# Kernel tuning notes

Hardware: AMD Instinct MI355X
Metric: run time of the kernel (lower is better)

## Reference

```python
import jax, jax.numpy as jnp
import numpy as np

N = 20000   # nodes
E = 320000  # edges
H = 4       # attention heads
GAT_SLOPE = 0.2   # DGL GATv2Conv internal leaky_relu slope
ACT_SLOPE = 0.01  # nn.LeakyReLU default slope


def gatv2_layer(h, src, dst, Wl, Wr, attn, b):
    """DGL GATv2Conv (share_weights=False, bias=True, eval mode).
    h: [N, Fin]; Wl/Wr: [Fin, H*D]; attn: [H, D]; b: [H*D]. Returns [N, H, D]."""
    n = h.shape[0]
    Hh, D = attn.shape
    fs = (h @ Wl).reshape(n, Hh, D)  # source projection
    fd = (h @ Wr).reshape(n, Hh, D)  # destination projection
    # edge-wise GATv2 score: a^T leaky_relu(Wl h_u + Wr h_v)
    e = jax.nn.leaky_relu(fs[src] + fd[dst], negative_slope=GAT_SLOPE)  # [E,H,D]
    logit = jnp.einsum('ehd,hd->eh', e, attn)  # [E,H]
    # edge softmax over incoming edges of each dst node (numerically stable)
    m = jax.ops.segment_max(logit, dst, num_segments=n)
    a = jnp.exp(logit - m[dst])
    s = jax.ops.segment_sum(a, dst, num_segments=n)
    alpha = a / s[dst]  # [E,H]
    out = jax.ops.segment_sum(alpha[:, :, None] * fs[src], dst, num_segments=n)
    return out + b.reshape(1, Hh, D)


def setup_inputs() -> dict:
    key = jax.random.key(0)
    ks = jax.random.split(key, 16)

    def w(k, shape, fan_in):
        return (jax.random.normal(k, shape, jnp.float32) / np.float32(np.sqrt(fan_in)))

    return {
        'n_feat': jax.random.normal(ks[0], (N, 512), jnp.float32),
        'src': jax.random.randint(ks[1], (E,), 0, N, jnp.int32),
        'dst': jax.random.randint(ks[2], (E,), 0, N, jnp.int32),
        # layer 0: 512 -> H x 128
        'Wl0': w(ks[3], (512, H * 128), 512), 'Wr0': w(ks[4], (512, H * 128), 512),
        'attn0': w(ks[5], (H, 128), 128), 'b0': jnp.zeros((H * 128,), jnp.float32),
        # layer 1: 128 -> H x 128
        'Wl1': w(ks[6], (128, H * 128), 128), 'Wr1': w(ks[7], (128, H * 128), 128),
        'attn1': w(ks[8], (H, 128), 128), 'b1': jnp.zeros((H * 128,), jnp.float32),
        # layer 2 (output): 128 -> H x 64
        'Wl2': w(ks[9], (128, H * 64), 128), 'Wr2': w(ks[10], (128, H * 64), 128),
        'attn2': w(ks[11], (H, 64), 64), 'b2': jnp.zeros((H * 64,), jnp.float32),
    }


def reference(n_feat, src, dst, Wl0, Wr0, attn0, b0, Wl1, Wr1, attn1, b1,
              Wl2, Wr2, attn2, b2):
    h = n_feat.reshape(n_feat.shape[0], -1)  # nn.Flatten
    for (Wl, Wr, attn, b) in ((Wl0, Wr0, attn0, b0),
                              (Wl1, Wr1, attn1, b1),
                              (Wl2, Wr2, attn2, b2)):
        h = gatv2_layer(h, src, dst, Wl, Wr, attn, b)  # [N,H,D]
        h = h.mean(axis=1)                              # head mean
        h = jax.nn.leaky_relu(h, negative_slope=ACT_SLOPE)
    # dgl.mean_nodes: per-graph mean readout (single graph -> [1, out])
    return h.mean(axis=0, keepdims=True)
```

## Files before the change

### kernel.cpp

```cpp
#include <hip/hip_runtime.h>
#include <hip/hip_bf16.h>
#include <stdint.h>


#define GAT_SLOPE 0.2f
#define ACT_SLOPE 0.01f
#define MAXDEG 64

typedef _Float16 half8 __attribute__((ext_vector_type(8)));
typedef _Float16 v2h __attribute__((ext_vector_type(2)));
typedef float floatx4 __attribute__((ext_vector_type(4)));

struct TransDesc {
  const float* src;
  _Float16* dst;
  int K, M, off;
};
struct PreArgs {
  TransDesc d[9];
  int wTotal;
  const float* nf;
  _Float16* A0;
  int aTotal;
  const int* src;
  const int* dst;
  int* counts;
  int* pcsrc;
  int E;
};

__global__ __launch_bounds__(256) void preproc_kernel(PreArgs pa) {
  int i = blockIdx.x * 256 + threadIdx.x;
  const int total = pa.wTotal + pa.aTotal + pa.E;
  if (i >= total) return;
  if (i < pa.wTotal) {
    int q = 0;
#pragma unroll
    for (int j = 1; j < 9; ++j)
      if (i >= pa.d[j].off) q = j;
    int local = i - pa.d[q].off;
    int K = pa.d[q].K, M = pa.d[q].M;
    int m = local / K, k = local % K;
    pa.d[q].dst[local] = (_Float16)pa.d[q].src[(size_t)k * M + m];
  } else if (i < pa.wTotal + pa.aTotal) {
    int j = i - pa.wTotal;
    pa.A0[j] = (_Float16)pa.nf[j];
  } else {
    int e = i - pa.wTotal - pa.aTotal;
    int d = pa.dst[e];
    int pos = atomicAdd(&pa.counts[d], 1);
    if (pos < MAXDEG) pa.pcsrc[(size_t)d * MAXDEG + pos] = pa.src[e];
  }
}

__device__ __forceinline__ void gload_lds16(const _Float16* g, _Float16* l) {
  __builtin_amdgcn_global_load_lds(
      (__attribute__((address_space(1))) unsigned int*)g,
      (__attribute__((address_space(3))) unsigned int*)l, 16, 0, 0);
}

#define TM 128
#define TN 128
#define TK 32

__global__ __launch_bounds__(256) void gemm_mfma_dual_kernel(
    const _Float16* __restrict__ A, const _Float16* __restrict__ B0,
    const _Float16* __restrict__ B1, _Float16* __restrict__ C0,
    _Float16* __restrict__ C1, int Nrow, int K, int M, int nStrips,
    int nbxLog2) {
  const int id = blockIdx.x;
  const int xcd = id & 7;
  const int s = id >> 3;
  const int nbx = 1 << nbxLog2;
  const int col = s & (nbx - 1);
  const int chunk = s >> nbxLog2;
  const int strip = chunk * 8 + xcd;
  if (strip >= nStrips) return;

  const int nb = nbx >> 1;
  const bool second = col >= nb;
  const _Float16* B = second ? B1 : B0;
  _Float16* C = second ? C1 : C0;
  const int bn = (second ? col - nb : col) * TN;
  const int bm = strip * TM;

  __shared__ __align__(16) _Float16 As[TM * TK];
  __shared__ __align__(16) _Float16 Bs[TN * TK];

  const int tid = threadIdx.x;
  const int w = tid >> 6;
  const int lane = tid & 63;
  const int wr = w >> 1;
  const int wc = w & 1;
  const int quad = lane >> 4;
  const int lr = lane & 15;

  const int lrow = lane >> 2;
  const int loff = (lane & 3) * 8;

  floatx4 acc[4][4];
#pragma unroll
  for (int i = 0; i < 4; ++i)
#pragma unroll
    for (int j = 0; j < 4; ++j) acc[i][j] = (floatx4){0.f, 0.f, 0.f, 0.f};

  const int KT = K / TK;
  for (int kt = 0; kt < KT; ++kt) {
    const int k0 = kt * TK;
#pragma unroll
    for (int half = 0; half < 2; ++half) {
      const int r0 = w * 32 + half * 16;
      int ga = bm + r0 + lrow;
      if (ga >= Nrow) ga = Nrow - 1;
      gload_lds16(A + (size_t)ga * K + k0 + loff, As + r0 * TK);
      gload_lds16(B + (size_t)(bn + r0 + lrow) * K + k0 + loff, Bs + r0 * TK);
    }
    __syncthreads();

    half8 ar[4], br[4];
#pragma unroll
    for (int i = 0; i < 4; ++i) {
      int row = wr * 64 + i * 16 + lr;
      ar[i] = *(const half8*)(As + row * TK + quad * 8);
    }
#pragma unroll
    for (int j = 0; j < 4; ++j) {
      int colr = wc * 64 + j * 16 + lr;
      br[j] = *(const half8*)(Bs + colr * TK + quad * 8);
    }
#pragma unroll
    for (int i = 0; i < 4; ++i)
#pragma unroll
      for (int j = 0; j < 4; ++j)
        acc[i][j] = __builtin_amdgcn_mfma_f32_16x16x32_f16(ar[i], br[j],
                                                           acc[i][j], 0, 0, 0);
    __syncthreads();
  }

#pragma unroll
  for (int i = 0; i < 4; ++i) {
#pragma unroll
    for (int r = 0; r < 4; ++r) {
      int row = bm + wr * 64 + i * 16 + quad * 4 + r;
      if (row >= Nrow) continue;
#pragma unroll
      for (int j = 0; j < 4; ++j) {
        int colc = bn + wc * 64 + j * 16 + lr;
        C[(size_t)row * M + colc] = (_Float16)acc[i][j][r];
      }
    }
  }
}

template <int CTRL>
__device__ __forceinline__ float dpp_add(float x) {
  int y = __builtin_amdgcn_update_dpp(0, __builtin_bit_cast(int, x), CTRL,
                                      0xF, 0xF, true);
  return x + __builtin_bit_cast(float, y);
}
__device__ __forceinline__ float row_sum16(float x) {
  x = dpp_add<0x121>(x);
  x = dpp_add<0x122>(x);
  x = dpp_add<0x124>(x);
  x = dpp_add<0x128>(x);
  return x;
}

template <int D>
__global__ __launch_bounds__(256) void node_attn_kernel(
    const _Float16* __restrict__ fs, const _Float16* __restrict__ fd,
    const int* __restrict__ counts, const int* __restrict__ pcsrc,
    const _Float16* __restrict__ attnT, const float* __restrict__ bias,
    float* __restrict__ hout, _Float16* __restrict__ oh, int N) {
  constexpr int HD = 4 * D;
  constexpr int R = HD / 64;
  constexpr int R2 = R / 2;
  typedef _Float16 halfR __attribute__((ext_vector_type(R)));
  union Frag {
    halfR v;
    v2h h[R2];
    _Float16 s[R];
  };
  const int wid = threadIdx.x >> 6;
  const int lane = threadIdx.x & 63;
  const int v = blockIdx.x * 4 + wid;
  if (v >= N) return;

  const v2h slope2 = {(_Float16)GAT_SLOPE, (_Float16)GAT_SLOPE};

  const int cnt = min(counts[v], MAXDEG);
  int idxReg = pcsrc[(size_t)v * MAXDEG + lane];
  Frag fdv;
  fdv.v = *(const halfR*)(fd + (size_t)v * HD + lane * R);
  Frag arf;
  arf.v = *(const halfR*)(attnT + lane * R);

  float m = -INFINITY, l = 0.f;
  float O[R];
#pragma unroll
  for (int i = 0; i < R; ++i) O[i] = 0.f;

  if (cnt > 0) {
    const int lastIdx = __builtin_amdgcn_readlane(idxReg, cnt - 1);
    const int nb = (cnt + 7) >> 3;

    auto loadb = [&](Frag* t, int base) {
#pragma unroll
      for (int q = 0; q < 8; ++q) {
        const int bq = base + q;
        const int sidx =
            (bq < cnt) ? __builtin_amdgcn_readlane(idxReg, bq) : lastIdx;
        t[q].v = *(const halfR*)(fs + (size_t)sidx * HD + lane * R);
      }
    };

    auto compute = [&](Frag* t, int base) {
      float p[8];
#pragma unroll
      for (int q = 0; q < 8; ++q) {
        float acc = 0.f;
#pragma unroll
        for (int j = 0; j < R2; ++j) {
          v2h x = t[q].h[j] + fdv.h[j];
          x = __builtin_elementwise_max(x, x * slope2);
          acc = __builtin_amdgcn_fdot2(arf.h[j], x, acc, false);
        }
        acc = row_sum16(acc);
        p[q] = (base + q < cnt) ? acc : -INFINITY;
      }
      float mnew = m;
#pragma unroll
      for (int q = 0; q < 8; ++q) mnew = fmaxf(mnew, p[q]);
      const float sc = __expf(m - mnew);
      float w[8];
      float wsum = 0.f;
#pragma unroll
      for (int q = 0; q < 8; ++q) {
        w[q] = __expf(p[q] - mnew);
        wsum += w[q];
      }
      l = l * sc + wsum;
#pragma unroll
      for (int i = 0; i < R; ++i) {
        float acc = (float)t[0].s[i] * w[0];
#pragma unroll
        for (int q = 1; q < 8; ++q) acc = fmaf((float)t[q].s[i], w[q], acc);
        O[i] = fmaf(O[i], sc, acc);
      }
      m = mnew;
    };

    Frag tA[8], tB[8];
    loadb(tA, 0);
    int bi = 0;
    for (;;) {
      if (bi + 1 < nb) loadb(tB, (bi + 1) * 8);
      compute(tA, bi * 8);
      ++bi;
      if (bi == nb) break;
      if (bi + 1 < nb) loadb(tA, (bi + 1) * 8);
      compute(tB, bi * 8);
      ++bi;
      if (bi == nb) break;
    }
  }

  const float inv = (l > 0.f) ? 1.f / l : 0.f;
#pragma unroll
  for (int i = 0; i < R; ++i) O[i] = O[i] * inv + bias[lane * R + i];
#pragma unroll
  for (int i = 0; i < R; ++i) {
    O[i] += __shfl_xor(O[i], 16, 64);
    O[i] += __shfl_xor(O[i], 32, 64);
    float x = O[i] * 0.25f;
    O[i] = x > 0.f ? x : x * ACT_SLOPE;
  }
  if (lane < 16) {
    const size_t base = (size_t)v * D + lane * R;
    if (hout) {
#pragma unroll
      for (int i = 0; i < R; ++i) hout[base + i] = O[i];
    }
    if (oh) {
#pragma unroll
      for (int i = 0; i < R; ++i) oh[base + i] = (_Float16)O[i];
    }
  }
}

__global__ __launch_bounds__(64) void final_mean_kernel(
    const float* __restrict__ h, float* __restrict__ out, int N) {
  const int d = threadIdx.x;
  float acc = 0.f;
  for (int n = blockIdx.x; n < N; n += gridDim.x) acc += h[(size_t)n * 64 + d];
  atomicAdd(&out[d], acc / (float)N);
}

extern "C" void kernel_launch(void* const* d_in, const int* in_sizes, int n_in,
                              void* d_out, int out_size, void* d_ws,
                              size_t ws_size, hipStream_t stream) {
  const float* n_feat = (const float*)d_in[0];
  const int* src = (const int*)d_in[1];
  const int* dst = (const int*)d_in[2];
  const float* Wl[3] = {(const float*)d_in[3], (const float*)d_in[7],
                        (const float*)d_in[11]};
  const float* Wr[3] = {(const float*)d_in[4], (const float*)d_in[8],
                        (const float*)d_in[12]};
  const float* attn[3] = {(const float*)d_in[5], (const float*)d_in[9],
                          (const float*)d_in[13]};
  const float* bias[3] = {(const float*)d_in[6], (const float*)d_in[10],
                          (const float*)d_in[14]};

  const int N = in_sizes[0] / 512;
  const int E = in_sizes[1];
  const int Kdim[3] = {512, 128, 128};
  const int Mdim[3] = {512, 512, 256};
  const int attnLen[3] = {512, 512, 256};

  char* ws = (char*)d_ws;
  size_t o = 0;
  auto alloc = [&](size_t bytes) {
    void* p = ws + o;
    o += (bytes + 15) & ~(size_t)15;
    return p;
  };
  _Float16* fs = (_Float16*)alloc((size_t)N * 512 * 2);
  _Float16* fd = (_Float16*)alloc((size_t)N * 512 * 2);
  _Float16* A0 = (_Float16*)alloc((size_t)N * 512 * 2);
  _Float16* h1 = (_Float16*)alloc((size_t)N * 128 * 2);
  _Float16* h2 = (_Float16*)alloc((size_t)N * 128 * 2);
  float* hfin = (float*)alloc((size_t)N * 64 * 4);
  _Float16 *WlT[3], *WrT[3], *attnT[3];
  for (int L = 0; L < 3; ++L) {
    size_t sz = (size_t)Kdim[L] * Mdim[L] * 2;
    WlT[L] = (_Float16*)alloc(sz);
    WrT[L] = (_Float16*)alloc(sz);
  }
  for (int L = 0; L < 3; ++L) attnT[L] = (_Float16*)alloc(attnLen[L] * 2);
  int* counts = (int*)alloc((size_t)N * 4);
  int* pcsrc = (int*)alloc((size_t)N * MAXDEG * 4);

  hipMemsetAsync(counts, 0, (size_t)N * sizeof(int), stream);
  {
    PreArgs pa;
    int off = 0;
    for (int L = 0; L < 3; ++L) {
      pa.d[2 * L] = {Wl[L], WlT[L], Kdim[L], Mdim[L], off};
      off += Kdim[L] * Mdim[L];
      pa.d[2 * L + 1] = {Wr[L], WrT[L], Kdim[L], Mdim[L], off};
      off += Kdim[L] * Mdim[L];
    }
    for (int L = 0; L < 3; ++L) {
      pa.d[6 + L] = {attn[L], attnT[L], attnLen[L], 1, off};
      off += attnLen[L];
    }
    pa.wTotal = off;
    pa.nf = n_feat;
    pa.A0 = A0;
    pa.aTotal = N * 512;
    pa.src = src;
    pa.dst = dst;
    pa.counts = counts;
    pa.pcsrc = pcsrc;
    pa.E = E;
    int total = pa.wTotal + pa.aTotal + pa.E;
    preproc_kernel<<<(total + 255) / 256, 256, 0, stream>>>(pa);
  }

  const _Float16* Ain[3] = {A0, h1, h2};

  const int nStrips = (N + TM - 1) / TM;
  const int S8 = ((nStrips + 7) / 8) * 8;

  const int attnGrid = (N + 3) / 4;

  for (int L = 0; L < 3; ++L) {
    const int K = Kdim[L], M = Mdim[L];
    const int nbx = 2 * M / TN;
    const int nbxLog2 = (nbx == 8) ? 3 : 2;
    gemm_mfma_dual_kernel<<<S8 * nbx, 256, 0, stream>>>(
        Ain[L], WlT[L], WrT[L], fs, fd, N, K, M, nStrips, nbxLog2);
    if (L == 0) {
      node_attn_kernel<128><<<attnGrid, 256, 0, stream>>>(
          fs, fd, counts, pcsrc, attnT[L], bias[L], nullptr, h1, N);
    } else if (L == 1) {
      node_attn_kernel<128><<<attnGrid, 256, 0, stream>>>(
          fs, fd, counts, pcsrc, attnT[L], bias[L], nullptr, h2, N);
    } else {
      node_attn_kernel<64><<<attnGrid, 256, 0, stream>>>(
          fs, fd, counts, pcsrc, attnT[L], bias[L], hfin, nullptr, N);
    }
  }

  hipMemsetAsync(d_out, 0, 64 * sizeof(float), stream);
  final_mean_kernel<<<256, 64, 0, stream>>>(hfin, (float*)d_out, N);
}
```

Before: 353.4 us.

## Split each node's edges across two waves with persistent grid-stride loop

The node attention kernel now runs two waves per block that each process half of one destination node's incoming edges with online softmax, then merge their partial max/sum/accumulators through shared memory. Blocks loop over nodes in grid-stride fashion and prefetch the next node's count, neighbor indices and destination features, and the gather batch shrinks from 8 to 4 rows with a scalar tail instead of padded lanes. The aim is to shorten the per-node serial chain, drop the padded-edge work, and cut register pressure. In exchange it adds a barrier per node and a shared-memory merge, and idles one wave during finalization.

```diff
diff --git a/kernel.cpp b/kernel.cpp
--- a/kernel.cpp
+++ b/kernel.cpp
@@ -167,7 +167,7 @@
 }
 
 template <int D>
-__global__ __launch_bounds__(256) void node_attn_kernel(
+__global__ __launch_bounds__(128) void node_attn_kernel(
     const _Float16* __restrict__ fs, const _Float16* __restrict__ fd,
     const int* __restrict__ counts, const int* __restrict__ pcsrc,
     const _Float16* __restrict__ attnT, const float* __restrict__ bias,
@@ -183,108 +183,187 @@
   };
   const int wid = threadIdx.x >> 6;
   const int lane = threadIdx.x & 63;
-  const int v = blockIdx.x * 4 + wid;
-  if (v >= N) return;
+
+  __shared__ float sO[2][64 * R];
+  __shared__ float sML[2][2][64];
 
   const v2h slope2 = {(_Float16)GAT_SLOPE, (_Float16)GAT_SLOPE};
-
-  const int cnt = min(counts[v], MAXDEG);
-  int idxReg = pcsrc[(size_t)v * MAXDEG + lane];
-  Frag fdv;
-  fdv.v = *(const halfR*)(fd + (size_t)v * HD + lane * R);
   Frag arf;
   arf.v = *(const halfR*)(attnT + lane * R);
 
-  float m = -INFINITY, l = 0.f;
-  float O[R];
-#pragma unroll
-  for (int i = 0; i < R; ++i) O[i] = 0.f;
-
-  if (cnt > 0) {
-    const int lastIdx = __builtin_amdgcn_readlane(idxReg, cnt - 1);
-    const int nb = (cnt + 7) >> 3;
-
-    auto loadb = [&](Frag* t, int base) {
-#pragma unroll
-      for (int q = 0; q < 8; ++q) {
-        const int bq = base + q;
-        const int sidx =
-            (bq < cnt) ? __builtin_amdgcn_readlane(idxReg, bq) : lastIdx;
+  int vcur = blockIdx.x;
+  int cnt_c = 0, idx_c = 0;
+  Frag fdv_c;
+  if (vcur < N) {
+    cnt_c = min(counts[vcur], MAXDEG);
+    idx_c = pcsrc[(size_t)vcur * MAXDEG + lane];
+    fdv_c.v = *(const halfR*)(fd + (size_t)vcur * HD + lane * R);
+  }
+
+  int parity = 0;
+  for (int v = blockIdx.x; v < N; v += gridDim.x, parity ^= 1) {
+    const int vn = v + gridDim.x;
+    int cnt_n = 0, idx_n = 0;
+    Frag fdv_n;
+    if (vn < N) {
+      cnt_n = min(counts[vn], MAXDEG);
+      idx_n = pcsrc[(size_t)vn * MAXDEG + lane];
+      fdv_n.v = *(const halfR*)(fd + (size_t)vn * HD + lane * R);
+    }
+
+    const int cnt = cnt_c;
+    const int idxv = idx_c;
+    const Frag fdvl = fdv_c;
+
+    float m = -INFINITY, l = 0.f;
+    float O[R];
+#pragma unroll
+    for (int i = 0; i < R; ++i) O[i] = 0.f;
+
+    const int mid = (cnt + 1) >> 1;
+    int k = wid ? mid : 0;
+    const int ke = wid ? cnt : mid;
+
+    auto loadb = [&](Frag* t, int kk) {
+#pragma unroll
+      for (int q = 0; q < 4; ++q) {
+        const int sidx = __builtin_amdgcn_readlane(idxv, kk + q);
         t[q].v = *(const halfR*)(fs + (size_t)sidx * HD + lane * R);
       }
     };
 
-    auto compute = [&](Frag* t, int base) {
-      float p[8];
-#pragma unroll
-      for (int q = 0; q < 8; ++q) {
-        float acc = 0.f;
-#pragma unroll
-        for (int j = 0; j < R2; ++j) {
-          v2h x = t[q].h[j] + fdv.h[j];
-          x = __builtin_elementwise_max(x, x * slope2);
-          acc = __builtin_amdgcn_fdot2(arf.h[j], x, acc, false);
-        }
-        acc = row_sum16(acc);
-        p[q] = (base + q < cnt) ? acc : -INFINITY;
-      }
-      float mnew = m;
-#pragma unroll
-      for (int q = 0; q < 8; ++q) mnew = fmaxf(mnew, p[q]);
+    auto compute4 = [&](Frag* t) {
+      float p0 = 0.f, p1 = 0.f, p2 = 0.f, p3 = 0.f;
+#pragma unroll
+      for (int j = 0; j < R2; ++j) {
+        v2h x0 = t[0].h[j] + fdvl.h[j];
+        v2h x1 = t[1].h[j] + fdvl.h[j];
+        v2h x2 = t[2].h[j] + fdvl.h[j];
+        v2h x3 = t[3].h[j] + fdvl.h[j];
+        x0 = __builtin_elementwise_max(x0, x0 * slope2);
+        x1 = __builtin_elementwise_max(x1, x1 * slope2);
+        x2 = __builtin_elementwise_max(x2, x2 * slope2);
+        x3 = __builtin_elementwise_max(x3, x3 * slope2);
+        p0 = __builtin_amdgcn_fdot2(arf.h[j], x0, p0, false);
+        p1 = __builtin_amdgcn_fdot2(arf.h[j], x1, p1, false);
+        p2 = __builtin_amdgcn_fdot2(arf.h[j], x2, p2, false);
+        p3 = __builtin_amdgcn_fdot2(arf.h[j], x3, p3, false);
+      }
+      p0 = row_sum16(p0);
+      p1 = row_sum16(p1);
+      p2 = row_sum16(p2);
+      p3 = row_sum16(p3);
+      const float mq = fmaxf(fmaxf(p0, p1), fmaxf(p2, p3));
+      const float mnew = fmaxf(m, mq);
       const float sc = __expf(m - mnew);
-      float w[8];
-      float wsum = 0.f;
-#pragma unroll
-      for (int q = 0; q < 8; ++q) {
-        w[q] = __expf(p[q] - mnew);
-        wsum += w[q];
-      }
-      l = l * sc + wsum;
+      const float w0 = __expf(p0 - mnew);
+      const float w1 = __expf(p1 - mnew);
+      const float w2 = __expf(p2 - mnew);
+      const float w3 = __expf(p3 - mnew);
+      l = l * sc + (w0 + w1 + w2 + w3);
 #pragma unroll
       for (int i = 0; i < R; ++i) {
-        float acc = (float)t[0].s[i] * w[0];
-#pragma unroll
-        for (int q = 1; q < 8; ++q) acc = fmaf((float)t[q].s[i], w[q], acc);
+        float acc = (float)t[0].s[i] * w0;
+        acc = fmaf((float)t[1].s[i], w1, acc);
+        acc = fmaf((float)t[2].s[i], w2, acc);
+        acc = fmaf((float)t[3].s[i], w3, acc);
         O[i] = fmaf(O[i], sc, acc);
       }
       m = mnew;
     };
 
-    Frag tA[8], tB[8];
-    loadb(tA, 0);
-    int bi = 0;
-    for (;;) {
-      if (bi + 1 < nb) loadb(tB, (bi + 1) * 8);
-      compute(tA, bi * 8);
-      ++bi;
-      if (bi == nb) break;
-      if (bi + 1 < nb) loadb(tA, (bi + 1) * 8);
-      compute(tB, bi * 8);
-      ++bi;
-      if (bi == nb) break;
-    }
-  }
-
-  const float inv = (l > 0.f) ? 1.f / l : 0.f;
-#pragma unroll
-  for (int i = 0; i < R; ++i) O[i] = O[i] * inv + bias[lane * R + i];
-#pragma unroll
-  for (int i = 0; i < R; ++i) {
-    O[i] += __shfl_xor(O[i], 16, 64);
-    O[i] += __shfl_xor(O[i], 32, 64);
-    float x = O[i] * 0.25f;
-    O[i] = x > 0.f ? x : x * ACT_SLOPE;
-  }
-  if (lane < 16) {
-    const size_t base = (size_t)v * D + lane * R;
-    if (hout) {
-#pragma unroll
-      for (int i = 0; i < R; ++i) hout[base + i] = O[i];
-    }
-    if (oh) {
-#pragma unroll
-      for (int i = 0; i < R; ++i) oh[base + i] = (_Float16)O[i];
-    }
+    {
+      const int nb = (ke - k) >> 2;
+      if (nb > 0) {
+        Frag tA[4], tB[4];
+        loadb(tA, k);
+        int bi = 0;
+        for (;;) {
+          if (bi + 1 < nb) loadb(tB, k + 4);
+          compute4(tA);
+          k += 4;
+          ++bi;
+          if (bi == nb) break;
+          if (bi + 1 < nb) loadb(tA, k + 4);
+          compute4(tB);
+          k += 4;
+          ++bi;
+          if (bi == nb) break;
+        }
+      }
+    }
+    for (; k < ke; ++k) {
+      const int sidx = __builtin_amdgcn_readlane(idxv, k);
+      Frag t0;
+      t0.v = *(const halfR*)(fs + (size_t)sidx * HD + lane * R);
+      float p0 = 0.f;
+#pragma unroll
+      for (int j = 0; j < R2; ++j) {
+        v2h x0 = t0.h[j] + fdvl.h[j];
+        x0 = __builtin_elementwise_max(x0, x0 * slope2);
+        p0 = __builtin_amdgcn_fdot2(arf.h[j], x0, p0, false);
+      }
+      p0 = row_sum16(p0);
+      const float mnew = fmaxf(m, p0);
+      const float sc = __expf(m - mnew);
+      const float p = __expf(p0 - mnew);
+      l = l * sc + p;
+#pragma unroll
+      for (int i = 0; i < R; ++i) O[i] = fmaf(O[i], sc, p * (float)t0.s[i]);
+      m = mnew;
+    }
+
+    if (wid == 1) {
+      sML[parity][0][lane] = m;
+      sML[parity][1][lane] = l;
+#pragma unroll
+      for (int i = 0; i < R; ++i) sO[parity][i * 64 + lane] = O[i];
+    }
+    __syncthreads();
+    if (wid == 0) {
+      const float m1 = sML[parity][0][lane];
+      const float l1 = sML[parity][1][lane];
+      const float mstar = fmaxf(m, m1);
+      const float a0 = (l > 0.f) ? __expf(m - mstar) : 0.f;
+      const float a1 = (l1 > 0.f) ? __expf(m1 - mstar) : 0.f;
+      l = l * a0 + l1 * a1;
+#pragma unroll
+      for (int i = 0; i < R; ++i) O[i] = O[i] * a0 + sO[parity][i * 64 + lane] * a1;
+
+      const float inv = (l > 0.f) ? 1.f / l : 0.f;
+      float biasv[R];
+#pragma unroll
+      for (int i = 0; i < R; i += 4) {
+        floatx4 b4 = *(const floatx4*)(bias + lane * R + i);
+        biasv[i] = b4[0];
+        biasv[i + 1] = b4[1];
+        biasv[i + 2] = b4[2];
+        biasv[i + 3] = b4[3];
+      }
+#pragma unroll
+      for (int i = 0; i < R; ++i) O[i] = O[i] * inv + biasv[i];
+#pragma unroll
+      for (int i = 0; i < R; ++i) {
+        O[i] += __shfl_xor(O[i], 16, 64);
+        O[i] += __shfl_xor(O[i], 32, 64);
+        float x = O[i] * 0.25f;
+        O[i] = x > 0.f ? x : x * ACT_SLOPE;
+      }
+      if (lane < 16) {
+        const size_t base = (size_t)v * D + lane * R;
+        if (hout) {
+#pragma unroll
+          for (int i = 0; i < R; ++i) hout[base + i] = O[i];
+        }
+        if (oh) {
+#pragma unroll
+          for (int i = 0; i < R; ++i) oh[base + i] = (_Float16)O[i];
+        }
+      }
+    }
+    cnt_c = cnt_n;
+    idx_c = idx_n;
+    fdv_c = fdv_n;
   }
 }
 
@@ -372,7 +451,7 @@
   const int nStrips = (N + TM - 1) / TM;
   const int S8 = ((nStrips + 7) / 8) * 8;
 
-  const int attnGrid = (N + 3) / 4;
+  const int attnGrid = (N + 7) / 8;
 
   for (int L = 0; L < 3; ++L) {
     const int K = Kdim[L], M = Mdim[L];
@@ -381,13 +460,13 @@
     gemm_mfma_dual_kernel<<<S8 * nbx, 256, 0, stream>>>(
         Ain[L], WlT[L], WrT[L], fs, fd, N, K, M, nStrips, nbxLog2);
     if (L == 0) {
-      node_attn_kernel<128><<<attnGrid, 256, 0, stream>>>(
+      node_attn_kernel<128><<<attnGrid, 128, 0, stream>>>(
           fs, fd, counts, pcsrc, attnT[L], bias[L], nullptr, h1, N);
     } else if (L == 1) {
-      node_attn_kernel<128><<<attnGrid, 256, 0, stream>>>(
+      node_attn_kernel<128><<<attnGrid, 128, 0, stream>>>(
           fs, fd, counts, pcsrc, attnT[L], bias[L], nullptr, h2, N);
     } else {
-      node_attn_kernel<64><<<attnGrid, 256, 0, stream>>>(
+      node_attn_kernel<64><<<attnGrid, 128, 0, stream>>>(
           fs, fd, counts, pcsrc, attnT[L], bias[L], hfin, nullptr, N);
     }
   }
```

New measurement: 366.9 us. 1.04x slower.
